# Optimization experiments

Hardware: AMD Instinct MI355X
Metric: run time of the kernel (lower is better)

The kernel has to match this reference:

```python
import jax, jax.numpy as jnp
import numpy as np

N = 4096            # reservoir size
MAX_DIM = 4608      # max_dynamic_reservoir_dim
INPUT_DIM = 1024
LEAK_RATE = 0.1
SPIKE_THRESHOLD = 0.5
T, B = 128, 128


def setup_inputs() -> dict:
    key = jax.random.key(0)
    k1, k2, k3, k4 = jax.random.split(key, 4)
    x = jax.random.normal(k1, (T, B, INPUT_DIM), dtype=jnp.float32)
    state0 = jnp.zeros((B, MAX_DIM), dtype=jnp.float32)
    # keras RandomNormal default stddev=0.05 for reservoir, 0.1 for input/gate
    W_res = 0.05 * jax.random.normal(k2, (N, N), dtype=jnp.float32)
    W_in = 0.1 * jax.random.normal(k3, (N, INPUT_DIM), dtype=jnp.float32)
    W_gate = 0.1 * jax.random.normal(k4, (3 * N, INPUT_DIM), dtype=jnp.float32)
    return {"x": x, "state0": state0, "W_res": W_res, "W_in": W_in, "W_gate": W_gate}


def _cell(prev_padded, x_t, W_res, W_in, W_gate):
    prev = prev_padded[:, :N]                                  # [B, N]
    input_part = x_t @ W_in.T                                  # [B, N]
    reservoir_part = prev @ W_res                              # [B, N]
    gate = jax.nn.sigmoid(x_t @ W_gate.T)                      # [B, 3N]
    i_gate, f_gate, o_gate = jnp.split(gate, 3, axis=-1)
    state = (1.0 - LEAK_RATE) * (f_gate * prev) \
            + LEAK_RATE * jnp.tanh(i_gate * (input_part + reservoir_part))
    state = o_gate * state
    state = jnp.where(state > SPIKE_THRESHOLD, state - SPIKE_THRESHOLD, state)
    padded = jnp.concatenate(
        [state, jnp.zeros((state.shape[0], MAX_DIM - N), dtype=state.dtype)], axis=1)
    return padded


def reference(x, state0, W_res, W_in, W_gate):
    def step(carry, x_t):
        new = _cell(carry, x_t, W_res, W_in, W_gate)
        return new, new
    _, outs = jax.lax.scan(step, state0, x)   # outs: [T, B, MAX_DIM]
    return outs
```

## Files before the change

kernel.cpp:

```cpp
#include <hip/hip_runtime.h>
#include <hip/hip_bf16.h>
#include <hip/hip_fp16.h>

#define N_RES   4096
#define MAXD    4608
#define IN_DIM  1024
#define T_STEPS 128
#define B_SZ    128

typedef __attribute__((ext_vector_type(8))) short bf16x8;
typedef __attribute__((ext_vector_type(8))) _Float16 f16x8;
typedef __attribute__((ext_vector_type(4))) float f32x4;

__device__ __forceinline__ short f2bf(float x) {
  union { float f; unsigned u; } v; v.f = x;
  unsigned r = v.u + 0x7fffu + ((v.u >> 16) & 1u);
  return (short)(r >> 16);
}
__device__ __forceinline__ short f2h(float x) {
  union { _Float16 h; short s; } u; u.h = (_Float16)x; return u.s;
}
__device__ __forceinline__ float h2f(short s) {
  union { _Float16 h; short s; } u; u.s = s; return (float)u.h;
}
__device__ __forceinline__ unsigned char f2fp8(float x) {
  return (unsigned char)(__builtin_amdgcn_cvt_pk_fp8_f32(x, 0.f, 0, false) & 0xff);
}

__device__ __forceinline__ void gload16(const void* g, void* l) {
  __builtin_amdgcn_global_load_lds(
      (const __attribute__((address_space(1))) void*)g,
      (__attribute__((address_space(3))) void*)l,
      16, 0, 0);
}

__global__ void k_zero_pad(float* __restrict__ out) {
  int row = blockIdx.x;
  int t = threadIdx.x;
  *(float4*)(out + (size_t)row * MAXD + N_RES + t * 4) = float4{0.f, 0.f, 0.f, 0.f};
}

__global__ void k_init_state(const float* __restrict__ s0,
                             float* __restrict__ sF, unsigned char* __restrict__ s8) {
  int i = blockIdx.x * 256 + threadIdx.x;
  int m = i >> 12, n = i & 4095;
  float v = s0[m * MAXD + n];
  sF[i] = v;
  s8[i] = f2fp8(v);
}

__global__ void k_wres_t(const float* __restrict__ W, unsigned char* __restrict__ bt) {
  __shared__ float tile[64][65];
  int k0 = blockIdx.y * 64, n0 = blockIdx.x * 64;
  int tx = threadIdx.x & 63, ty = threadIdx.x >> 6;
  #pragma unroll
  for (int r = 0; r < 64; r += 4)
    tile[r + ty][tx] = W[(long)(k0 + r + ty) * N_RES + n0 + tx];
  __syncthreads();
  #pragma unroll
  for (int r = 0; r < 64; r += 4)
    bt[(long)(n0 + r + ty) * N_RES + k0 + tx] = f2fp8(tile[tx][r + ty]);
}

__global__ void k_build_b2(const float* __restrict__ Win,
                           const float* __restrict__ Wg, short* __restrict__ B2) {
  int r = blockIdx.x;
  const float* src = (r < N_RES) ? (Win + (long)r * IN_DIM)
                                 : (Wg + (long)(r - N_RES) * IN_DIM);
  short* dst = B2 + (long)r * IN_DIM;
  for (int c = threadIdx.x; c < IN_DIM; c += 256)
    dst[c] = f2h(src[c]);
}

__global__ void k_build_a2(const float* __restrict__ x, short* __restrict__ A2, int t0) {
  int r = blockIdx.x;
  const float* src = x + (long)(t0 * B_SZ + r) * IN_DIM;
  short* dst = A2 + (long)r * IN_DIM;
  for (int c = threadIdx.x; c < IN_DIM; c += 256)
    dst[c] = f2h(src[c]);
}

__global__ __launch_bounds__(512, 2) void k_gemm_pre(
    const short* __restrict__ A2, const short* __restrict__ B2,
    _Float16* __restrict__ ip, unsigned char* __restrict__ gates, int Mrows) {
  __shared__ short lA[2][2][128 * 64];
  __shared__ short lB[2][2][128 * 64];
  int tid = threadIdx.x, lane = tid & 63, wid = tid >> 6;
  int wr = wid >> 2, wc = wid & 3;

  int nwg = gridDim.x, orig = blockIdx.x;
  int mtiles = nwg >> 6;
  int mt, nt;
  if ((mtiles & 3) == 0) {
    int xcd = orig & 7, idx = orig >> 3;
    int w = idx & 31, sq = idx >> 5;
    nt = xcd * 8 + (w & 7);
    mt = sq * 4 + (w >> 3);
  } else {
    int qx = nwg >> 3, rx = nwg & 7, xcd = orig & 7;
    int wgid = (xcd < rx ? xcd * (qx + 1) : rx * (qx + 1) + (xcd - rx) * qx) + (orig >> 3);
    mt = wgid >> 6; nt = wgid & 63;
  }
  long m0 = (long)mt * 256, n0 = (long)nt * 256;
  long mclamp = Mrows - 1;

  int c0 = tid, c1 = 512 + tid;
  int r0 = c0 >> 3, r1 = c1 >> 3;
  int cc0 = ((c0 & 7) ^ (r0 & 7)) * 8, cc1 = ((c1 & 7) ^ (r1 & 7)) * 8;

  const short *pA00, *pA01, *pA10, *pA11, *pB00, *pB01, *pB10, *pB11;
  {
    long a00 = m0 + r0;       if (a00 > mclamp) a00 = mclamp;
    long a01 = m0 + r1;       if (a01 > mclamp) a01 = mclamp;
    long a10 = m0 + 128 + r0; if (a10 > mclamp) a10 = mclamp;
    long a11 = m0 + 128 + r1; if (a11 > mclamp) a11 = mclamp;
    pA00 = A2 + a00 * IN_DIM + cc0;  pA01 = A2 + a01 * IN_DIM + cc1;
    pA10 = A2 + a10 * IN_DIM + cc0;  pA11 = A2 + a11 * IN_DIM + cc1;
    pB00 = B2 + (n0 + r0) * IN_DIM + cc0;        pB01 = B2 + (n0 + r1) * IN_DIM + cc1;
    pB10 = B2 + (n0 + 128 + r0) * IN_DIM + cc0;  pB11 = B2 + (n0 + 128 + r1) * IN_DIM + cc1;
  }

  #define STG_A0(kt, b) { gload16(pA00 + (kt)*64, &lA[b][0][c0*8]); gload16(pA01 + (kt)*64, &lA[b][0][c1*8]); }
  #define STG_A1(kt, b) { gload16(pA10 + (kt)*64, &lA[b][1][c0*8]); gload16(pA11 + (kt)*64, &lA[b][1][c1*8]); }
  #define STG_B0(kt, b) { gload16(pB00 + (kt)*64, &lB[b][0][c0*8]); gload16(pB01 + (kt)*64, &lB[b][0][c1*8]); }
  #define STG_B1(kt, b) { gload16(pB10 + (kt)*64, &lB[b][1][c0*8]); gload16(pB11 + (kt)*64, &lB[b][1][c1*8]); }

  int lm = lane & 15;
  int colS0 = ((lane >> 4) * 8) ^ ((lane & 7) << 3);
  int colS1 = (32 + (lane >> 4) * 8) ^ ((lane & 7) << 3);
  int arow[4], brow[2];
  #pragma unroll
  for (int i = 0; i < 4; ++i) arow[i] = (wr * 64 + i * 16 + lm) * 64;
  #pragma unroll
  for (int j = 0; j < 2; ++j) brow[j] = (wc * 32 + j * 16 + lm) * 64;

  f16x8 aF[4][2], bFh[2][2][2];
  f32x4 acc[2][4][4] = {};

  #define RD_A(qm, b) { _Pragma("unroll") for (int i = 0; i < 4; ++i) {        \
      aF[i][0] = *(const f16x8*)&lA[b][qm][arow[i] + colS0];                   \
      aF[i][1] = *(const f16x8*)&lA[b][qm][arow[i] + colS1]; } }
  #define RD_B(h, b) { _Pragma("unroll") for (int j = 0; j < 2; ++j) {         \
      bFh[h][j][0] = *(const f16x8*)&lB[b][h][brow[j] + colS0];                \
      bFh[h][j][1] = *(const f16x8*)&lB[b][h][brow[j] + colS1]; } }
  #define MM(qm, qn) { __builtin_amdgcn_s_setprio(1);                          \
      _Pragma("unroll") for (int i = 0; i < 4; ++i)                            \
      _Pragma("unroll") for (int j = 0; j < 2; ++j) {                          \
        acc[qm][i][(qn)*2+j] = __builtin_amdgcn_mfma_f32_16x16x32_f16(         \
            aF[i][0], bFh[qn][j][0], acc[qm][i][(qn)*2+j], 0, 0, 0);           \
        acc[qm][i][(qn)*2+j] = __builtin_amdgcn_mfma_f32_16x16x32_f16(         \
            aF[i][1], bFh[qn][j][1], acc[qm][i][(qn)*2+j], 0, 0, 0); }         \
      __builtin_amdgcn_s_setprio(0); }

  STG_A0(0, 0); STG_B0(0, 0); STG_B1(0, 0); STG_A1(0, 0);

  const int nk = IN_DIM / 64;
  for (int kt = 0; kt < nk; ++kt) {
    int buf = kt & 1, nbuf = buf ^ 1;
    int ktn = (kt + 1 < nk) ? kt + 1 : kt;
    asm volatile("s_waitcnt vmcnt(4)\n\ts_barrier" ::: "memory");
    RD_A(0, buf); RD_B(0, buf);
    STG_A0(ktn, nbuf);
    MM(0, 0);
    asm volatile("s_barrier" ::: "memory");
    asm volatile("s_waitcnt vmcnt(4)\n\ts_barrier" ::: "memory");
    RD_B(1, buf);
    STG_B0(ktn, nbuf);
    MM(0, 1);
    asm volatile("s_barrier" ::: "memory");
    asm volatile("s_waitcnt vmcnt(4)\n\ts_barrier" ::: "memory");
    RD_A(1, buf);
    STG_B1(ktn, nbuf);
    MM(1, 0);
    asm volatile("s_barrier" ::: "memory");
    STG_A1(ktn, nbuf);
    MM(1, 1);
    asm volatile("s_barrier" ::: "memory");
  }
  #undef STG_A0
  #undef STG_A1
  #undef STG_B0
  #undef STG_B1
  #undef RD_A
  #undef RD_B
  #undef MM

  #pragma unroll
  for (int qm = 0; qm < 2; ++qm)
    #pragma unroll
    for (int i = 0; i < 4; ++i)
      #pragma unroll
      for (int qn = 0; qn < 2; ++qn)
        #pragma unroll
        for (int j = 0; j < 2; ++j)
          #pragma unroll
          for (int q = 0; q < 4; ++q) {
            long m = m0 + qm * 128 + wr * 64 + i * 16 + (lane >> 4) * 4 + q;
            long n = n0 + qn * 128 + wc * 32 + j * 16 + lm;
            if (m >= Mrows) continue;
            float v = acc[qm][i][qn * 2 + j][q];
            if (n < N_RES) {
              ip[m * N_RES + n] = (_Float16)v;
            } else {
              float g = 1.f / (1.f + __expf(-v));
              gates[m * 12288 + (n - N_RES)] = (unsigned char)(g * 255.f + 0.5f);
            }
          }
}

__global__ __launch_bounds__(512) void k_step_gemm(
    const unsigned char* __restrict__ A8,
    const unsigned char* __restrict__ B8,
    short* __restrict__ part) {
  __shared__ unsigned char lA[3][64 * 256];
  __shared__ unsigned char lB[3][128 * 256];
  int tid = threadIdx.x, lane = tid & 63, wid = tid >> 6;
  int wm = wid >> 2, wn = wid & 3;

  int b = blockIdx.x;
  int xcd = b & 7, i2 = b >> 3;
  int m_h = i2 & 1, kc = (i2 >> 1) & 3, n_tl = i2 >> 3;
  int n_t = xcd * 4 + n_tl;
  int m0 = m_h * 64, n0 = n_t * 128, kb = kc * 1024;

  const unsigned char* pA[2];
  const unsigned char* pB[4];
  #pragma unroll
  for (int i = 0; i < 2; ++i) {
    int c = i * 512 + tid, row = c >> 4;
    pA[i] = A8 + (size_t)(m0 + row) * N_RES + kb + (((c & 15) ^ (row & 7)) * 16);
  }
  #pragma unroll
  for (int i = 0; i < 4; ++i) {
    int c = i * 512 + tid, row = c >> 4;
    pB[i] = B8 + (size_t)(n0 + row) * N_RES + kb + (((c & 15) ^ (row & 7)) * 16);
  }

  #define STAGE(kt, bi) { int k0s = (kt) * 256;                                \
    _Pragma("unroll") for (int i = 0; i < 2; ++i)                              \
      gload16(pA[i] + k0s, &lA[bi][(i * 512 + tid) * 16]);                     \
    _Pragma("unroll") for (int i = 0; i < 4; ++i)                              \
      gload16(pB[i] + k0s, &lB[bi][(i * 512 + tid) * 16]); }

  f32x4 acc[2][2] = {};

  #define COMPUTE(bi)                                                          \
    { _Pragma("unroll")                                                        \
      for (int kk = 0; kk < 256; kk += 32) {                                   \
        int colS = (kk + (lane >> 4) * 8) ^ ((lane & 7) << 4);                 \
        long aF0 = *(const long*)&lA[bi][(wm * 32 + (lane & 15)) * 256 + colS];      \
        long aF1 = *(const long*)&lA[bi][(wm * 32 + 16 + (lane & 15)) * 256 + colS]; \
        long bF0 = *(const long*)&lB[bi][(wn * 32 + (lane & 15)) * 256 + colS];      \
        long bF1 = *(const long*)&lB[bi][(wn * 32 + 16 + (lane & 15)) * 256 + colS]; \
        acc[0][0] = __builtin_amdgcn_mfma_f32_16x16x32_fp8_fp8(aF0, bF0, acc[0][0], 0, 0, 0); \
        acc[0][1] = __builtin_amdgcn_mfma_f32_16x16x32_fp8_fp8(aF0, bF1, acc[0][1], 0, 0, 0); \
        acc[1][0] = __builtin_amdgcn_mfma_f32_16x16x32_fp8_fp8(aF1, bF0, acc[1][0], 0, 0, 0); \
        acc[1][1] = __builtin_amdgcn_mfma_f32_16x16x32_fp8_fp8(aF1, bF1, acc[1][1], 0, 0, 0); \
      } }

  STAGE(0, 0);
  STAGE(1, 1);

  int bi = 0, sb = 2;
  for (int kt = 0; kt < 3; ++kt) {
    asm volatile("s_waitcnt vmcnt(6)" ::: "memory");
    __builtin_amdgcn_s_barrier();
    if (kt < 2) STAGE(kt + 2, sb);
    COMPUTE(bi);
    ++bi; if (bi == 3) bi = 0;
    ++sb; if (sb == 3) sb = 0;
  }
  asm volatile("s_waitcnt vmcnt(0)" ::: "memory");
  __builtin_amdgcn_s_barrier();
  COMPUTE(bi);
  #undef STAGE
  #undef COMPUTE

  short* dst = part + (size_t)kc * (B_SZ * N_RES);
  #pragma unroll
  for (int i = 0; i < 2; ++i)
    #pragma unroll
    for (int j = 0; j < 2; ++j)
      #pragma unroll
      for (int q = 0; q < 4; ++q) {
        int m = m0 + wm * 32 + i * 16 + (lane >> 4) * 4 + q;
        int n = n0 + wn * 32 + j * 16 + (lane & 15);
        dst[(size_t)m * N_RES + n] = f2h(acc[i][j][q]);
      }
}

__global__ void k_step_red(
    const short* __restrict__ part,
    const _Float16* __restrict__ ip,
    const unsigned char* __restrict__ gt,
    float* __restrict__ sF,
    unsigned char* __restrict__ s8w,
    float* __restrict__ out) {
  int e = (blockIdx.x * 256 + threadIdx.x) * 4;
  int m = e >> 12, n = e & 4095;
  float res[4] = {0.f, 0.f, 0.f, 0.f};
  #pragma unroll
  for (int k = 0; k < 4; ++k) {
    short4 p = *(const short4*)(part + ((size_t)k << 19) + e);
    res[0] += h2f(p.x); res[1] += h2f(p.y); res[2] += h2f(p.z); res[3] += h2f(p.w);
  }
  short4 ipr = *(const short4*)((const short*)ip + e);
  const unsigned char* g = gt + (size_t)m * 12288 + n;
  uchar4 igr = *(const uchar4*)g;
  uchar4 fgr = *(const uchar4*)(g + 4096);
  uchar4 ogr = *(const uchar4*)(g + 8192);
  float4 pr = *(const float4*)(sF + e);

  float prv[4] = { pr.x, pr.y, pr.z, pr.w };
  short ipa[4] = { ipr.x, ipr.y, ipr.z, ipr.w };
  unsigned char iga[4] = { igr.x, igr.y, igr.z, igr.w };
  unsigned char fga[4] = { fgr.x, fgr.y, fgr.z, fgr.w };
  unsigned char oga[4] = { ogr.x, ogr.y, ogr.z, ogr.w };

  const float is = 1.f / 255.f;
  float so[4];
  unsigned char s8[4];
  #pragma unroll
  for (int q = 0; q < 4; ++q) {
    float s = 0.9f * ((float)fga[q] * is * prv[q])
            + 0.1f * tanhf((float)iga[q] * is * (h2f(ipa[q]) + res[q]));
    s = (float)oga[q] * is * s;
    if (s > 0.5f) s -= 0.5f;
    so[q] = s;
    s8[q] = f2fp8(s);
  }
  *(float4*)(out + (size_t)m * MAXD + n) = float4{so[0], so[1], so[2], so[3]};
  *(float4*)(sF + e) = float4{so[0], so[1], so[2], so[3]};
  *(uchar4*)(s8w + e) = uchar4{s8[0], s8[1], s8[2], s8[3]};
}

extern "C" void kernel_launch(void* const* d_in, const int* in_sizes, int n_in,
                              void* d_out, int out_size, void* d_ws, size_t ws_size,
                              hipStream_t stream) {
  const float* x      = (const float*)d_in[0];
  const float* state0 = (const float*)d_in[1];
  const float* W_res  = (const float*)d_in[2];
  const float* W_in   = (const float*)d_in[3];
  const float* W_gate = (const float*)d_in[4];
  float* out = (float*)d_out;
  char* ws = (char*)d_ws;

  size_t off = 0;
  unsigned char* WresBT8 = (unsigned char*)(ws + off); off += (size_t)N_RES * N_RES;
  short* B2     = (short*)(ws + off); off += (size_t)16384 * IN_DIM * 2;
  float* sF     = (float*)(ws + off); off += (size_t)B_SZ * N_RES * 4;
  unsigned char* s8_0 = (unsigned char*)(ws + off); off += (size_t)B_SZ * N_RES;
  unsigned char* s8_1 = (unsigned char*)(ws + off); off += (size_t)B_SZ * N_RES;
  short* part   = (short*)(ws + off); off += (size_t)4 * B_SZ * N_RES * 2;
  size_t fixed = off;
  size_t per = (size_t)B_SZ * IN_DIM * 2 + (size_t)B_SZ * N_RES * 2 + (size_t)B_SZ * 12288;

  int Tc = T_STEPS;
  while (Tc > 1 && fixed + (size_t)Tc * per > ws_size) Tc >>= 1;

  short*          A2  = (short*)(ws + fixed);
  _Float16*       ipb = (_Float16*)(ws + fixed + (size_t)Tc * B_SZ * IN_DIM * 2);
  unsigned char*  gtb = (unsigned char*)(ws + fixed + (size_t)Tc * B_SZ * IN_DIM * 2
                                         + (size_t)Tc * B_SZ * N_RES * 2);

  k_zero_pad<<<T_STEPS * B_SZ, 128, 0, stream>>>(out);
  k_init_state<<<(B_SZ * N_RES) / 256, 256, 0, stream>>>(state0, sF, s8_0);
  k_wres_t<<<dim3(64, 64), 256, 0, stream>>>(W_res, WresBT8);
  k_build_b2<<<16384, 256, 0, stream>>>(W_in, W_gate, B2);

  for (int t0 = 0; t0 < T_STEPS; t0 += Tc) {
    k_build_a2<<<Tc * B_SZ, 256, 0, stream>>>(x, A2, t0);
    int Mrows = Tc * B_SZ;
    int mtiles = (Mrows + 255) / 256;
    k_gemm_pre<<<mtiles * 64, 512, 0, stream>>>(A2, B2, ipb, gtb, Mrows);
    for (int tl = 0; tl < Tc; ++tl) {
      int t = t0 + tl;
      const unsigned char* Ar = (t & 1) ? s8_1 : s8_0;
      unsigned char*       Aw = (t & 1) ? s8_0 : s8_1;
      k_step_gemm<<<256, 512, 0, stream>>>(Ar, WresBT8, part);
      k_step_red<<<512, 256, 0, stream>>>(
          part,
          ipb + (size_t)tl * B_SZ * N_RES,
          gtb + (size_t)tl * B_SZ * 12288,
          sF, Aw,
          out + (size_t)t * B_SZ * MAXD);
    }
  }
}
```

Before: 2.419 ms.

## Fuse per-step split-K reduction into GEMM via last-block atomic counter

Result: slower. 4.597 ms (+90.1%).

```diff
diff --git a/kernel.cpp b/kernel.cpp
--- a/kernel.cpp
+++ b/kernel.cpp
@@ -38,6 +38,10 @@
   int row = blockIdx.x;
   int t = threadIdx.x;
   *(float4*)(out + (size_t)row * MAXD + N_RES + t * 4) = float4{0.f, 0.f, 0.f, 0.f};
+}
+
+__global__ void k_zero_cnt(int* __restrict__ cnt) {
+  cnt[threadIdx.x] = 0;
 }
 
 __global__ void k_init_state(const float* __restrict__ s0,
@@ -208,12 +212,19 @@
           }
 }
 
-__global__ __launch_bounds__(512) void k_step_gemm(
+__global__ __launch_bounds__(512) void k_step_fused(
     const unsigned char* __restrict__ A8,
     const unsigned char* __restrict__ B8,
-    short* __restrict__ part) {
+    short* __restrict__ part,
+    const _Float16* __restrict__ ip,
+    const unsigned char* __restrict__ gt,
+    float* __restrict__ sF,
+    unsigned char* __restrict__ s8w,
+    float* __restrict__ out,
+    int* __restrict__ cnt) {
   __shared__ unsigned char lA[3][64 * 256];
   __shared__ unsigned char lB[3][128 * 256];
+  __shared__ int sDone;
   int tid = threadIdx.x, lane = tid & 63, wid = tid >> 6;
   int wm = wid >> 2, wn = wid & 3;
 
@@ -222,6 +233,7 @@
   int m_h = i2 & 1, kc = (i2 >> 1) & 3, n_tl = i2 >> 3;
   int n_t = xcd * 4 + n_tl;
   int m0 = m_h * 64, n0 = n_t * 128, kb = kc * 1024;
+  int region = m_h * 32 + n_t;
 
   const unsigned char* pA[2];
   const unsigned char* pB[4];
@@ -287,51 +299,62 @@
         int n = n0 + wn * 32 + j * 16 + (lane & 15);
         dst[(size_t)m * N_RES + n] = f2h(acc[i][j][q]);
       }
-}
-
-__global__ void k_step_red(
-    const short* __restrict__ part,
-    const _Float16* __restrict__ ip,
-    const unsigned char* __restrict__ gt,
-    float* __restrict__ sF,
-    unsigned char* __restrict__ s8w,
-    float* __restrict__ out) {
-  int e = (blockIdx.x * 256 + threadIdx.x) * 4;
-  int m = e >> 12, n = e & 4095;
-  float res[4] = {0.f, 0.f, 0.f, 0.f};
-  #pragma unroll
-  for (int k = 0; k < 4; ++k) {
-    short4 p = *(const short4*)(part + ((size_t)k << 19) + e);
-    res[0] += h2f(p.x); res[1] += h2f(p.y); res[2] += h2f(p.z); res[3] += h2f(p.w);
-  }
-  short4 ipr = *(const short4*)((const short*)ip + e);
-  const unsigned char* g = gt + (size_t)m * 12288 + n;
-  uchar4 igr = *(const uchar4*)g;
-  uchar4 fgr = *(const uchar4*)(g + 4096);
-  uchar4 ogr = *(const uchar4*)(g + 8192);
-  float4 pr = *(const float4*)(sF + e);
-
-  float prv[4] = { pr.x, pr.y, pr.z, pr.w };
-  short ipa[4] = { ipr.x, ipr.y, ipr.z, ipr.w };
-  unsigned char iga[4] = { igr.x, igr.y, igr.z, igr.w };
-  unsigned char fga[4] = { fgr.x, fgr.y, fgr.z, fgr.w };
-  unsigned char oga[4] = { ogr.x, ogr.y, ogr.z, ogr.w };
-
+
+  __syncthreads();
+  if (tid == 0) {
+    __threadfence();
+    int prev = atomicAdd(&cnt[region], 1);
+    sDone = (prev == 3);
+    if (prev == 3) cnt[region] = 0;
+  }
+  __syncthreads();
+  if (!sDone) return;
+
+  __threadfence();
   const float is = 1.f / 255.f;
-  float so[4];
-  unsigned char s8[4];
-  #pragma unroll
-  for (int q = 0; q < 4; ++q) {
-    float s = 0.9f * ((float)fga[q] * is * prv[q])
-            + 0.1f * tanhf((float)iga[q] * is * (h2f(ipa[q]) + res[q]));
-    s = (float)oga[q] * is * s;
-    if (s > 0.5f) s -= 0.5f;
-    so[q] = s;
-    s8[q] = f2fp8(s);
-  }
-  *(float4*)(out + (size_t)m * MAXD + n) = float4{so[0], so[1], so[2], so[3]};
-  *(float4*)(sF + e) = float4{so[0], so[1], so[2], so[3]};
-  *(uchar4*)(s8w + e) = uchar4{s8[0], s8[1], s8[2], s8[3]};
+  #pragma unroll
+  for (int v = 0; v < 4; ++v) {
+    int slot = v * 512 + tid;
+    int mloc = slot >> 5;
+    int nloc = (slot & 31) * 4;
+    int m = m0 + mloc;
+    int n = n0 + nloc;
+    size_t e = (size_t)m * N_RES + n;
+
+    float res[4] = {0.f, 0.f, 0.f, 0.f};
+    #pragma unroll
+    for (int k2 = 0; k2 < 4; ++k2) {
+      short4 p = *(const short4*)(part + ((size_t)k2 << 19) + e);
+      res[0] += h2f(p.x); res[1] += h2f(p.y); res[2] += h2f(p.z); res[3] += h2f(p.w);
+    }
+    short4 ipr = *(const short4*)((const short*)ip + e);
+    const unsigned char* g = gt + (size_t)m * 12288 + n;
+    uchar4 igr = *(const uchar4*)g;
+    uchar4 fgr = *(const uchar4*)(g + 4096);
+    uchar4 ogr = *(const uchar4*)(g + 8192);
+    float4 pr = *(const float4*)(sF + e);
+
+    float prv[4] = { pr.x, pr.y, pr.z, pr.w };
+    short ipa[4] = { ipr.x, ipr.y, ipr.z, ipr.w };
+    unsigned char iga[4] = { igr.x, igr.y, igr.z, igr.w };
+    unsigned char fga[4] = { fgr.x, fgr.y, fgr.z, fgr.w };
+    unsigned char oga[4] = { ogr.x, ogr.y, ogr.z, ogr.w };
+
+    float so[4];
+    unsigned char s8[4];
+    #pragma unroll
+    for (int q = 0; q < 4; ++q) {
+      float s = 0.9f * ((float)fga[q] * is * prv[q])
+              + 0.1f * tanhf((float)iga[q] * is * (h2f(ipa[q]) + res[q]));
+      s = (float)oga[q] * is * s;
+      if (s > 0.5f) s -= 0.5f;
+      so[q] = s;
+      s8[q] = f2fp8(s);
+    }
+    *(float4*)(out + (size_t)m * MAXD + n) = float4{so[0], so[1], so[2], so[3]};
+    *(float4*)(sF + e) = float4{so[0], so[1], so[2], so[3]};
+    *(uchar4*)(s8w + e) = uchar4{s8[0], s8[1], s8[2], s8[3]};
+  }
 }
 
 extern "C" void kernel_launch(void* const* d_in, const int* in_sizes, int n_in,
@@ -352,6 +375,8 @@
   unsigned char* s8_0 = (unsigned char*)(ws + off); off += (size_t)B_SZ * N_RES;
   unsigned char* s8_1 = (unsigned char*)(ws + off); off += (size_t)B_SZ * N_RES;
   short* part   = (short*)(ws + off); off += (size_t)4 * B_SZ * N_RES * 2;
+  int*   cnt    = (int*)(ws + off);   off += 64 * sizeof(int);
+  off = (off + 255) & ~(size_t)255;
   size_t fixed = off;
   size_t per = (size_t)B_SZ * IN_DIM * 2 + (size_t)B_SZ * N_RES * 2 + (size_t)B_SZ * 12288;
 
@@ -364,6 +389,7 @@
                                          + (size_t)Tc * B_SZ * N_RES * 2);
 
   k_zero_pad<<<T_STEPS * B_SZ, 128, 0, stream>>>(out);
+  k_zero_cnt<<<1, 64, 0, stream>>>(cnt);
   k_init_state<<<(B_SZ * N_RES) / 256, 256, 0, stream>>>(state0, sF, s8_0);
   k_wres_t<<<dim3(64, 64), 256, 0, stream>>>(W_res, WresBT8);
   k_build_b2<<<16384, 256, 0, stream>>>(W_in, W_gate, B2);
@@ -377,13 +403,13 @@
       int t = t0 + tl;
       const unsigned char* Ar = (t & 1) ? s8_1 : s8_0;
       unsigned char*       Aw = (t & 1) ? s8_0 : s8_1;
-      k_step_gemm<<<256, 512, 0, stream>>>(Ar, WresBT8, part);
-      k_step_red<<<512, 256, 0, stream>>>(
-          part,
+      k_step_fused<<<256, 512, 0, stream>>>(
+          Ar, WresBT8, part,
           ipb + (size_t)tl * B_SZ * N_RES,
           gtb + (size_t)tl * B_SZ * 12288,
           sF, Aw,
-          out + (size_t)t * B_SZ * MAXD);
+          out + (size_t)t * B_SZ * MAXD,
+          cnt);
     }
   }
 }
```
